# Kernel tuning notes

Measured on AMD Instinct MI355X. Metric: run time of the kernel, lower is better.

## Reference

```python
import jax, jax.numpy as jnp
import numpy as np

H = 12  # max_heads

def setup_inputs() -> dict:
    key = jax.random.key(0)
    ks = jax.random.split(key, 5)
    B, N, E = 8, 1024, 768
    return {
        "x": jax.random.normal(ks[0], (B, N, E), dtype=jnp.float32),
        "w_qkv": jax.random.normal(ks[1], (3 * E, E), dtype=jnp.float32) * 0.02,
        "b_qkv": jax.random.normal(ks[2], (3 * E,), dtype=jnp.float32) * 0.02,
        "w_proj": jax.random.normal(ks[3], (E, E), dtype=jnp.float32) * 0.02,
        "b_proj": jax.random.normal(ks[4], (E,), dtype=jnp.float32) * 0.02,
        "active_heads": 8,
    }

def reference(x, w_qkv, b_qkv, w_proj, b_proj, active_heads):
    B, N, E = x.shape
    D = E // H
    scale = D ** -0.5
    # qkv projection: [B,N,3E] -> [3,B,H,N,D]
    qkv = (x @ w_qkv.T + b_qkv).reshape(B, N, 3, H, D)
    qkv = jnp.transpose(qkv, (2, 0, 3, 1, 4))
    q, k, v = qkv[0], qkv[1], qkv[2]
    # head mask from active_heads (static int)
    head_mask = (jnp.arange(H) < active_heads).astype(x.dtype)
    m = head_mask[None, :, None, None]
    q = q * m
    k = k * m
    v = v * m
    attn = jax.nn.softmax(jnp.einsum("bhqd,bhkd->bhqk", q, k) * scale, axis=-1)
    out = jnp.einsum("bhqk,bhkd->bhqd", attn, v)
    out = jnp.transpose(out, (0, 2, 1, 3)).reshape(B, N, E)
    channel_mask = jnp.repeat(head_mask, D)  # [E]
    out = out * channel_mask[None, None, :]
    return out @ w_proj.T + b_proj
```

## Files before the change

### kernel.cpp

```cpp
#include <hip/hip_runtime.h>
#include <hip/hip_fp16.h>

#define NH 12
#define BSZ 8
#define NSEQ 1024
#define EDIM 768
#define DH 64

typedef _Float16 f16;
typedef f16 half8 __attribute__((ext_vector_type(8)));
typedef f16 half4 __attribute__((ext_vector_type(4)));
typedef float f32x4 __attribute__((ext_vector_type(4)));
typedef unsigned int u32;
typedef u32 u32x4 __attribute__((ext_vector_type(4)));

static __device__ __forceinline__ void gload16(const void* g, void* l) {
    __builtin_amdgcn_global_load_lds((const __attribute__((address_space(1))) u32*)g,
                                     (__attribute__((address_space(3))) u32*)l, 16, 0, 0);
}
static __device__ __forceinline__ u32 pkrtz(float a, float b) {
    auto h = __builtin_amdgcn_cvt_pkrtz(a, b);
    return __builtin_bit_cast(u32, h);
}
#define SHFU(v, s) ((u32)__shfl((int)(v), (s)))
#define MFMA16(a, b, c) __builtin_amdgcn_mfma_f32_16x16x32_f16((a), (b), (c), 0, 0, 0)

__global__ void cvt_all_kernel(const float* __restrict__ x, const float* __restrict__ wq,
                               const float* __restrict__ wp, f16* __restrict__ dst) {
    const int NX = BSZ * NSEQ * EDIM;
    const int NWQ = 3 * EDIM * EDIM;
    int i = (blockIdx.x * blockDim.x + threadIdx.x) * 4;
    const float* s;
    int j;
    if (i < NX) { s = x; j = i; }
    else if (i < NX + NWQ) { s = wq; j = i - NX; }
    else { s = wp; j = i - NX - NWQ; }
    float4 v = *(const float4*)(s + j);
    half4 o = { (f16)v.x, (f16)v.y, (f16)v.z, (f16)v.w };
    *(half4*)(dst + i) = o;
}

template<int MODE>
__global__ __launch_bounds__(256) void gemm_kernel(
    const f16* __restrict__ A, const f16* __restrict__ Wt, const float* __restrict__ bias,
    f16* __restrict__ qbuf, f16* __restrict__ kbuf, f16* __restrict__ vbuf,
    float* __restrict__ outp, const int* __restrict__ activep, int K, int NC)
{
    __shared__ __align__(16) f16 Ah[2][128][32];
    __shared__ __align__(16) f16 Bh[2][128][32];

    const int tid = threadIdx.x;
    const int c0 = blockIdx.x * 128;
    const int m0 = blockIdx.y * 128;
    if (MODE == 0) {
        int hb = (c0 % EDIM) >> 6;
        if (hb >= *activep) return;
    }
    const int lane = tid & 63;
    const int wid  = tid >> 6;
    const int wr = wid >> 1, wc = wid & 1;
    const int r16 = lane & 15, rg = lane >> 4;

    f32x4 acc[4][4];
#pragma unroll
    for (int i = 0; i < 4; ++i)
#pragma unroll
        for (int j = 0; j < 4; ++j)
            acc[i][j] = f32x4{0.f, 0.f, 0.f, 0.f};

    const int srow = wid * 32 + (lane >> 2);
    const int scol = (lane & 3) * 8;
    const f16* gA = A  + (size_t)(m0 + srow) * K + scol;
    const f16* gB = Wt + (size_t)(c0 + srow) * K + scol;
    const int nkt = K / 32;

    auto stage = [&](int buf, int kt) {
        const f16* a0 = gA + kt * 32;
        const f16* b0 = gB + kt * 32;
        gload16(a0,                  &Ah[buf][wid * 32][0]);
        gload16(a0 + (size_t)16 * K, &Ah[buf][wid * 32 + 16][0]);
        gload16(b0,                  &Bh[buf][wid * 32][0]);
        gload16(b0 + (size_t)16 * K, &Bh[buf][wid * 32 + 16][0]);
    };

    stage(0, 0);
    __syncthreads();
    int cur = 0;
    for (int kt = 0; kt < nkt; ++kt) {
        if (kt + 1 < nkt) stage(cur ^ 1, kt + 1);
        half8 af[4], bf[4];
#pragma unroll
        for (int f = 0; f < 4; ++f) {
            af[f] = *(const half8*)&Ah[cur][wr * 64 + f * 16 + r16][rg * 8];
            bf[f] = *(const half8*)&Bh[cur][wc * 64 + f * 16 + r16][rg * 8];
        }
#pragma unroll
        for (int fm = 0; fm < 4; ++fm)
#pragma unroll
            for (int fn = 0; fn < 4; ++fn)
                acc[fm][fn] = MFMA16(af[fm], bf[fn], acc[fm][fn]);
        __syncthreads();
        cur ^= 1;
    }

#pragma unroll
    for (int fn = 0; fn < 4; ++fn) {
        const int c = c0 + wc * 64 + fn * 16 + r16;
        const float bv = bias[c];
#pragma unroll
        for (int fm = 0; fm < 4; ++fm) {
            const int mbase = m0 + wr * 64 + fm * 16 + rg * 4;
#pragma unroll
            for (int r = 0; r < 4; ++r) {
                const float val = acc[fm][fn][r] + bv;
                const int m = mbase + r;
                if (MODE == 1) {
                    outp[(size_t)m * EDIM + c] = val;
                } else {
                    const int s  = c / EDIM;
                    const int cc = c % EDIM;
                    const int hh = cc >> 6, d = cc & 63;
                    const int bb = m >> 10, n = m & 1023;
                    f16* dst = (s == 0) ? qbuf : ((s == 1) ? kbuf : vbuf);
                    dst[(((size_t)bb * NH + hh) * NSEQ + n) * DH + d] = (f16)val;
                }
            }
        }
    }
}

__global__ __launch_bounds__(256) void attn_kernel(
    const f16* __restrict__ qbuf, const f16* __restrict__ kbuf, const f16* __restrict__ vbuf,
    f16* __restrict__ ctx, const int* __restrict__ activep)
{
    __shared__ __align__(16) f16 Kh[2][64][72];
    __shared__ __align__(16) f16 Vt[2][64][72];

    const int b = blockIdx.z, h = blockIdx.y;
    const int q0 = blockIdx.x * 64;
    const int tid = threadIdx.x, lane = tid & 63, wid = tid >> 6;

    if (h >= *activep) {
        const int r = tid >> 2, cp = tid & 3;
        half8 z = { (f16)0,(f16)0,(f16)0,(f16)0,(f16)0,(f16)0,(f16)0,(f16)0 };
        size_t base = ((size_t)b * NSEQ + q0 + r) * EDIM + h * DH + cp * 16;
        *(half8*)&ctx[base]     = z;
        *(half8*)&ctx[base + 8] = z;
        return;
    }

    const size_t hb = (((size_t)b * NH + h) * NSEQ) * DH;
    const f16* Q  = qbuf + hb;
    const f16* Kp = kbuf + hb;
    const f16* Vp = vbuf + hb;

    const int ql = lane & 15;
    const int g  = lane >> 4;

    half8 qb0, qb1;
    {
        const f16* qp = Q + (size_t)(q0 + wid * 16 + ql) * DH + g * 8;
        qb0 = *(const half8*)qp        * (f16)0.125f;
        qb1 = *(const half8*)(qp + 32) * (f16)0.125f;
    }

    const int krow = tid >> 2, kcol = (tid & 3) * 16;
    const f16* gK = Kp + (size_t)krow * DH + kcol;
    const f16* gV = Vp + (size_t)lane * DH + wid * 16;

    half8 kr0, kr1, vv0, vv1;
    auto loadT = [&](int kt) {
        const f16* pk = gK + (size_t)kt * 64 * DH;
        kr0 = *(const half8*)pk;
        kr1 = *(const half8*)(pk + 8);
        const f16* pv = gV + (size_t)kt * 64 * DH;
        vv0 = *(const half8*)pv;
        vv1 = *(const half8*)(pv + 8);
    };
    auto storeT = [&](int buf) {
        *(half8*)&Kh[buf][krow][kcol]     = kr0;
        *(half8*)&Kh[buf][krow][kcol + 8] = kr1;
#pragma unroll
        for (int j = 0; j < 8; ++j) {
            Vt[buf][wid * 16 + j][lane]     = vv0[j];
            Vt[buf][wid * 16 + 8 + j][lane] = vv1[j];
        }
    };

    loadT(0);
    storeT(0);

    f32x4 oacc[4];
#pragma unroll
    for (int i = 0; i < 4; ++i) oacc[i] = f32x4{0.f, 0.f, 0.f, 0.f};
    float mr = -INFINITY, lr = 0.f;

    const int src0 = ql + ((lane & 16) << 1);
    const int src1 = src0 + 16;
    const bool hi = (lane >= 32);

    for (int kt = 0; kt < NSEQ / 64; ++kt) {
        const int cur = kt & 1;
        if (kt + 1 < NSEQ / 64) loadT(kt + 1);
        __syncthreads();

        f32x4 st[4];
#pragma unroll
        for (int s = 0; s < 4; ++s) {
            f32x4 t = f32x4{0.f, 0.f, 0.f, 0.f};
            t = MFMA16(*(const half8*)&Kh[cur][s * 16 + ql][g * 8],      qb0, t);
            t = MFMA16(*(const half8*)&Kh[cur][s * 16 + ql][32 + g * 8], qb1, t);
            st[s] = t;
        }

        float pmax;
        {
            float m0v = fmaxf(fmaxf(st[0][0], st[0][1]), fmaxf(st[0][2], st[0][3]));
            float m1v = fmaxf(fmaxf(st[1][0], st[1][1]), fmaxf(st[1][2], st[1][3]));
            float m2v = fmaxf(fmaxf(st[2][0], st[2][1]), fmaxf(st[2][2], st[2][3]));
            float m3v = fmaxf(fmaxf(st[3][0], st[3][1]), fmaxf(st[3][2], st[3][3]));
            pmax = fmaxf(fmaxf(m0v, m1v), fmaxf(m2v, m3v));
        }
        pmax = fmaxf(pmax, __shfl_xor(pmax, 16));
        pmax = fmaxf(pmax, __shfl_xor(pmax, 32));
        const float mnew = fmaxf(mr, pmax);
        const float sc = __expf(mr - mnew);
        float psum = 0.f;
#pragma unroll
        for (int s = 0; s < 4; ++s)
#pragma unroll
            for (int r = 0; r < 4; ++r) {
                float p = __expf(st[s][r] - mnew);
                st[s][r] = p;
                psum += p;
            }
        psum += __shfl_xor(psum, 16);
        psum += __shfl_xor(psum, 32);
        lr = lr * sc + psum;
        mr = mnew;

#pragma unroll
        for (int r = 0; r < 4; ++r) {
            const float scr = __shfl(sc, (g << 2) | r);
            oacc[0][r] *= scr; oacc[1][r] *= scr; oacc[2][r] *= scr; oacc[3][r] *= scr;
        }

        const u32 w00 = pkrtz(st[0][0], st[0][1]), w01 = pkrtz(st[0][2], st[0][3]);
        const u32 w10 = pkrtz(st[1][0], st[1][1]), w11 = pkrtz(st[1][2], st[1][3]);
        const u32 w20 = pkrtz(st[2][0], st[2][1]), w21 = pkrtz(st[2][2], st[2][3]);
        const u32 w30 = pkrtz(st[3][0], st[3][1]), w31 = pkrtz(st[3][2], st[3][3]);

        u32x4 pa0, pa1;
        {
            u32 a, bb2;
            a = SHFU(w00, src0); bb2 = SHFU(w10, src0); pa0[0] = hi ? bb2 : a;
            a = SHFU(w01, src0); bb2 = SHFU(w11, src0); pa0[1] = hi ? bb2 : a;
            a = SHFU(w00, src1); bb2 = SHFU(w10, src1); pa0[2] = hi ? bb2 : a;
            a = SHFU(w01, src1); bb2 = SHFU(w11, src1); pa0[3] = hi ? bb2 : a;
            a = SHFU(w20, src0); bb2 = SHFU(w30, src0); pa1[0] = hi ? bb2 : a;
            a = SHFU(w21, src0); bb2 = SHFU(w31, src0); pa1[1] = hi ? bb2 : a;
            a = SHFU(w20, src1); bb2 = SHFU(w30, src1); pa1[2] = hi ? bb2 : a;
            a = SHFU(w21, src1); bb2 = SHFU(w31, src1); pa1[3] = hi ? bb2 : a;
        }
        const half8 pah0 = __builtin_bit_cast(half8, pa0);
        const half8 pah1 = __builtin_bit_cast(half8, pa1);

#pragma unroll
        for (int db = 0; db < 4; ++db) {
            oacc[db] = MFMA16(pah0, *(const half8*)&Vt[cur][db * 16 + ql][g * 8],      oacc[db]);
            oacc[db] = MFMA16(pah1, *(const half8*)&Vt[cur][db * 16 + ql][32 + g * 8], oacc[db]);
        }

        if (kt + 1 < NSEQ / 64) storeT(cur ^ 1);
    }

#pragma unroll
    for (int r = 0; r < 4; ++r) {
        const float li = 1.0f / __shfl(lr, (g << 2) | r);
        const int n = q0 + wid * 16 + (g << 2) + r;
#pragma unroll
        for (int db = 0; db < 4; ++db)
            ctx[((size_t)b * NSEQ + n) * EDIM + h * DH + db * 16 + ql] = (f16)(oacc[db][r] * li);
    }
}

extern "C" void kernel_launch(void* const* d_in, const int* in_sizes, int n_in,
                              void* d_out, int out_size, void* d_ws, size_t ws_size,
                              hipStream_t stream) {
    const float* x      = (const float*)d_in[0];
    const float* w_qkv  = (const float*)d_in[1];
    const float* b_qkv  = (const float*)d_in[2];
    const float* w_proj = (const float*)d_in[3];
    const float* b_proj = (const float*)d_in[4];
    const int*   active = (const int*)d_in[5];
    float* out = (float*)d_out;

    char* ws = (char*)d_ws;
    const size_t n_x  = (size_t)BSZ * NSEQ * EDIM;
    const size_t n_wq = (size_t)3 * EDIM * EDIM;
    const size_t n_wp = (size_t)EDIM * EDIM;
    const size_t n_hd = (size_t)BSZ * NH * NSEQ * DH;

    f16* xh   = (f16*)ws;
    f16* wqh  = xh + n_x;
    f16* wph  = wqh + n_wq;
    f16* qh   = wph + n_wp;
    f16* kh   = qh + n_hd;
    f16* vh   = kh + n_hd;
    f16* ctxh = vh + n_hd;

    const size_t n_cvt = n_x + n_wq + n_wp;
    cvt_all_kernel<<<(int)(n_cvt / 4 / 256), 256, 0, stream>>>(x, w_qkv, w_proj, xh);

    gemm_kernel<0><<<dim3(3 * EDIM / 128, BSZ * NSEQ / 128), 256, 0, stream>>>(
        xh, wqh, b_qkv, qh, kh, vh, nullptr, active, EDIM, 3 * EDIM);

    attn_kernel<<<dim3(NSEQ / 64, NH, BSZ), 256, 0, stream>>>(qh, kh, vh, ctxh, active);

    gemm_kernel<1><<<dim3(EDIM / 128, BSZ * NSEQ / 128), 256, 0, stream>>>(
        ctxh, wph, b_proj, nullptr, nullptr, nullptr, out, active, EDIM, EDIM);
}
```

Before: 132.3 us.

## Pre-transpose V, stage K/V via async global-to-LDS loads with XOR swizzle

```diff
diff --git a/kernel.cpp b/kernel.cpp
--- a/kernel.cpp
+++ b/kernel.cpp
@@ -12,7 +12,7 @@
 typedef f16 half4 __attribute__((ext_vector_type(4)));
 typedef float f32x4 __attribute__((ext_vector_type(4)));
 typedef unsigned int u32;
-typedef u32 u32x4 __attribute__((ext_vector_type(4)));
+typedef u32 u32x2 __attribute__((ext_vector_type(2)));
 
 static __device__ __forceinline__ void gload16(const void* g, void* l) {
     __builtin_amdgcn_global_load_lds((const __attribute__((address_space(1))) u32*)g,
@@ -22,7 +22,6 @@
     auto h = __builtin_amdgcn_cvt_pkrtz(a, b);
     return __builtin_bit_cast(u32, h);
 }
-#define SHFU(v, s) ((u32)__shfl((int)(v), (s)))
 #define MFMA16(a, b, c) __builtin_amdgcn_mfma_f32_16x16x32_f16((a), (b), (c), 0, 0, 0)
 
 __global__ void cvt_all_kernel(const float* __restrict__ x, const float* __restrict__ wq,
@@ -129,12 +128,38 @@
     }
 }
 
+__global__ __launch_bounds__(256) void vtrans_kernel(const f16* __restrict__ vbuf,
+                                                     f16* __restrict__ vtb,
+                                                     const int* __restrict__ activep) {
+    const int b = blockIdx.z, h = blockIdx.y;
+    if (h >= *activep) return;
+    const int n0 = blockIdx.x * 64;
+    __shared__ __align__(16) f16 T[64][72];
+    const f16* src = vbuf + (((size_t)b * NH + h) * NSEQ + n0) * DH;
+    f16* dst = vtb + ((size_t)b * NH + h) * DH * NSEQ;
+    const int t = threadIdx.x;
+    const int rn = t >> 2, rc = t & 3;
+    *(half8*)&T[rn][rc * 16]     = *(const half8*)&src[(size_t)rn * DH + rc * 16];
+    *(half8*)&T[rn][rc * 16 + 8] = *(const half8*)&src[(size_t)rn * DH + rc * 16 + 8];
+    __syncthreads();
+    const int d = t >> 2, nc = (t & 3) * 16;
+    half8 o0, o1;
+#pragma unroll
+    for (int j = 0; j < 8; ++j) {
+        o0[j] = T[nc + j][d];
+        o1[j] = T[nc + 8 + j][d];
+    }
+    *(half8*)&dst[(size_t)d * NSEQ + n0 + nc]     = o0;
+    *(half8*)&dst[(size_t)d * NSEQ + n0 + nc + 8] = o1;
+}
+
 __global__ __launch_bounds__(256) void attn_kernel(
-    const f16* __restrict__ qbuf, const f16* __restrict__ kbuf, const f16* __restrict__ vbuf,
+    const f16* __restrict__ qbuf, const f16* __restrict__ kbuf, const f16* __restrict__ vtb,
     f16* __restrict__ ctx, const int* __restrict__ activep)
 {
-    __shared__ __align__(16) f16 Kh[2][64][72];
-    __shared__ __align__(16) f16 Vt[2][64][72];
+    __shared__ __align__(16) f16 Kh[2][64][64];
+    __shared__ __align__(16) f16 Vh[2][64][64];
+    __shared__ __align__(16) f16 Ph[4][16][64];
 
     const int b = blockIdx.z, h = blockIdx.y;
     const int q0 = blockIdx.x * 64;
@@ -151,11 +176,12 @@
 
     const size_t hb = (((size_t)b * NH + h) * NSEQ) * DH;
     const f16* Q  = qbuf + hb;
-    const f16* Kp = kbuf + hb;
-    const f16* Vp = vbuf + hb;
+    const char* Kp = (const char*)(kbuf + hb);
+    const char* Vp = (const char*)(vtb + hb);
 
     const int ql = lane & 15;
     const int g  = lane >> 4;
+    const int q7 = ql & 7;
 
     half8 qb0, qb1;
     {
@@ -164,54 +190,44 @@
         qb1 = *(const half8*)(qp + 32) * (f16)0.125f;
     }
 
-    const int krow = tid >> 2, kcol = (tid & 3) * 16;
-    const f16* gK = Kp + (size_t)krow * DH + kcol;
-    const f16* gV = Vp + (size_t)lane * DH + wid * 16;
-
-    half8 kr0, kr1, vv0, vv1;
-    auto loadT = [&](int kt) {
-        const f16* pk = gK + (size_t)kt * 64 * DH;
-        kr0 = *(const half8*)pk;
-        kr1 = *(const half8*)(pk + 8);
-        const f16* pv = gV + (size_t)kt * 64 * DH;
-        vv0 = *(const half8*)pv;
-        vv1 = *(const half8*)(pv + 8);
+    const int srow8 = lane >> 3;
+    const int schk  = (lane & 7) ^ srow8;
+
+    auto stage = [&](int buf, int kt) {
+        const char* kb = Kp + (size_t)kt * 8192;
+#pragma unroll
+        for (int i = 0; i < 2; ++i) {
+            const int r = wid * 16 + i * 8 + srow8;
+            gload16(kb + (size_t)r * 128 + schk * 16, &Kh[buf][wid * 16 + i * 8][0]);
+            gload16(Vp + (size_t)r * (NSEQ * 2) + (size_t)kt * 128 + schk * 16,
+                    &Vh[buf][wid * 16 + i * 8][0]);
+        }
     };
-    auto storeT = [&](int buf) {
-        *(half8*)&Kh[buf][krow][kcol]     = kr0;
-        *(half8*)&Kh[buf][krow][kcol + 8] = kr1;
-#pragma unroll
-        for (int j = 0; j < 8; ++j) {
-            Vt[buf][wid * 16 + j][lane]     = vv0[j];
-            Vt[buf][wid * 16 + 8 + j][lane] = vv1[j];
-        }
-    };
-
-    loadT(0);
-    storeT(0);
 
     f32x4 oacc[4];
 #pragma unroll
     for (int i = 0; i < 4; ++i) oacc[i] = f32x4{0.f, 0.f, 0.f, 0.f};
     float mr = -INFINITY, lr = 0.f;
 
-    const int src0 = ql + ((lane & 16) << 1);
-    const int src1 = src0 + 16;
-    const bool hi = (lane >= 32);
-
-    for (int kt = 0; kt < NSEQ / 64; ++kt) {
+    char* prow = (char*)&Ph[wid][ql][0];
+
+    stage(0, 0);
+    const int NT = NSEQ / 64;
+    for (int kt = 0; kt < NT; ++kt) {
         const int cur = kt & 1;
-        if (kt + 1 < NSEQ / 64) loadT(kt + 1);
         __syncthreads();
+        if (kt + 1 < NT) stage(cur ^ 1, kt + 1);
 
         f32x4 st[4];
+        __builtin_amdgcn_s_setprio(1);
 #pragma unroll
         for (int s = 0; s < 4; ++s) {
             f32x4 t = f32x4{0.f, 0.f, 0.f, 0.f};
-            t = MFMA16(*(const half8*)&Kh[cur][s * 16 + ql][g * 8],      qb0, t);
-            t = MFMA16(*(const half8*)&Kh[cur][s * 16 + ql][32 + g * 8], qb1, t);
+            t = MFMA16(*(const half8*)((const char*)&Kh[cur][16 * s + ql][0] + ((g ^ q7) << 4)),       qb0, t);
+            t = MFMA16(*(const half8*)((const char*)&Kh[cur][16 * s + ql][0] + (((4 | g) ^ q7) << 4)), qb1, t);
             st[s] = t;
         }
+        __builtin_amdgcn_s_setprio(0);
 
         float pmax;
         {
@@ -245,33 +261,21 @@
             oacc[0][r] *= scr; oacc[1][r] *= scr; oacc[2][r] *= scr; oacc[3][r] *= scr;
         }
 
-        const u32 w00 = pkrtz(st[0][0], st[0][1]), w01 = pkrtz(st[0][2], st[0][3]);
-        const u32 w10 = pkrtz(st[1][0], st[1][1]), w11 = pkrtz(st[1][2], st[1][3]);
-        const u32 w20 = pkrtz(st[2][0], st[2][1]), w21 = pkrtz(st[2][2], st[2][3]);
-        const u32 w30 = pkrtz(st[3][0], st[3][1]), w31 = pkrtz(st[3][2], st[3][3]);
-
-        u32x4 pa0, pa1;
-        {
-            u32 a, bb2;
-            a = SHFU(w00, src0); bb2 = SHFU(w10, src0); pa0[0] = hi ? bb2 : a;
-            a = SHFU(w01, src0); bb2 = SHFU(w11, src0); pa0[1] = hi ? bb2 : a;
-            a = SHFU(w00, src1); bb2 = SHFU(w10, src1); pa0[2] = hi ? bb2 : a;
-            a = SHFU(w01, src1); bb2 = SHFU(w11, src1); pa0[3] = hi ? bb2 : a;
-            a = SHFU(w20, src0); bb2 = SHFU(w30, src0); pa1[0] = hi ? bb2 : a;
-            a = SHFU(w21, src0); bb2 = SHFU(w31, src0); pa1[1] = hi ? bb2 : a;
-            a = SHFU(w20, src1); bb2 = SHFU(w30, src1); pa1[2] = hi ? bb2 : a;
-            a = SHFU(w21, src1); bb2 = SHFU(w31, src1); pa1[3] = hi ? bb2 : a;
-        }
-        const half8 pah0 = __builtin_bit_cast(half8, pa0);
-        const half8 pah1 = __builtin_bit_cast(half8, pa1);
-
+#pragma unroll
+        for (int s = 0; s < 4; ++s) {
+            u32x2 w = { pkrtz(st[s][0], st[s][1]), pkrtz(st[s][2], st[s][3]) };
+            *(u32x2*)(prow + ((32 * s + 8 * g) ^ (q7 << 4))) = w;
+        }
+        const half8 pa0 = *(const half8*)(prow + ((16 * g) ^ (q7 << 4)));
+        const half8 pa1 = *(const half8*)(prow + ((64 + 16 * g) ^ (q7 << 4)));
+
+        __builtin_amdgcn_s_setprio(1);
 #pragma unroll
         for (int db = 0; db < 4; ++db) {
-            oacc[db] = MFMA16(pah0, *(const half8*)&Vt[cur][db * 16 + ql][g * 8],      oacc[db]);
-            oacc[db] = MFMA16(pah1, *(const half8*)&Vt[cur][db * 16 + ql][32 + g * 8], oacc[db]);
-        }
-
-        if (kt + 1 < NSEQ / 64) storeT(cur ^ 1);
+            oacc[db] = MFMA16(pa0, *(const half8*)((const char*)&Vh[cur][16 * db + ql][0] + ((g ^ q7) << 4)),       oacc[db]);
+            oacc[db] = MFMA16(pa1, *(const half8*)((const char*)&Vh[cur][16 * db + ql][0] + (((4 | g) ^ q7) << 4)), oacc[db]);
+        }
+        __builtin_amdgcn_s_setprio(0);
     }
 
 #pragma unroll
@@ -308,6 +312,7 @@
     f16* kh   = qh + n_hd;
     f16* vh   = kh + n_hd;
     f16* ctxh = vh + n_hd;
+    f16* vtb  = xh;
 
     const size_t n_cvt = n_x + n_wq + n_wp;
     cvt_all_kernel<<<(int)(n_cvt / 4 / 256), 256, 0, stream>>>(x, w_qkv, w_proj, xh);
@@ -315,7 +320,9 @@
     gemm_kernel<0><<<dim3(3 * EDIM / 128, BSZ * NSEQ / 128), 256, 0, stream>>>(
         xh, wqh, b_qkv, qh, kh, vh, nullptr, active, EDIM, 3 * EDIM);
 
-    attn_kernel<<<dim3(NSEQ / 64, NH, BSZ), 256, 0, stream>>>(qh, kh, vh, ctxh, active);
+    vtrans_kernel<<<dim3(NSEQ / 64, NH, BSZ), 256, 0, stream>>>(vh, vtb, active);
+
+    attn_kernel<<<dim3(NSEQ / 64, NH, BSZ), 256, 0, stream>>>(qh, kh, vtb, ctxh, active);
 
     gemm_kernel<1><<<dim3(EDIM / 128, BSZ * NSEQ / 128), 256, 0, stream>>>(
         ctxh, wph, b_proj, nullptr, nullptr, nullptr, out, active, EDIM, EDIM);
```

New measurement: 129.2 us. -2.3%, faster.
